# Kernel tuning notes

Hardware: AMD Instinct MI355X
Metric: run time of the kernel (lower is better)

Reference implementation:

```python
import jax, jax.numpy as jnp
import numpy as np

B, L_Q, L_K = 16, 256, 256
Q_DIM, K_DIM, H_DIM, V_DIM = 256, 256, 128, 128


def setup_inputs() -> dict:
    key = jax.random.key(0)
    k1, k2, k3, k4, k5, k6 = jax.random.split(key, 6)
    query = jax.random.normal(k1, (B, L_Q, Q_DIM), dtype=jnp.float32)
    key_t = jax.random.normal(k2, (B, L_K, K_DIM), dtype=jnp.float32)
    value = jax.random.normal(k3, (B, L_Q, V_DIM), dtype=jnp.float32)
    # Linear weights stored as [in, out] for x @ W (equivalent to torch Linear, no bias)
    Wq = jax.random.normal(k4, (Q_DIM, H_DIM), dtype=jnp.float32) / np.sqrt(Q_DIM)
    Wk = jax.random.normal(k5, (K_DIM, H_DIM), dtype=jnp.float32) / np.sqrt(K_DIM)
    v = jax.random.uniform(k6, (H_DIM,), dtype=jnp.float32, minval=-0.1, maxval=0.1)
    return {"query": query, "key": key_t, "value": value, "Wq": Wq, "Wk": Wk, "v": v}


def reference(query, key, value, Wq, Wk, v):
    # Project first (equivalent to applying Linear after the expand, but cheaper):
    qp = jnp.einsum("bqd,dh->bqh", query, Wq)  # [B, l_q, h]
    kp = jnp.einsum("bkd,dh->bkh", key, Wk)    # [B, l_k, h]
    # score[b, k, q] = tanh(qp[b,q] + kp[b,k]) . v  -> [B, l_k, l_q]
    score = jnp.einsum("bkqh,h->bkq", jnp.tanh(qp[:, None, :, :] + kp[:, :, None, :]), v)
    attention = jax.nn.softmax(score, axis=-1)  # softmax over query positions (dim -1)
    context = jnp.einsum("bkq,bqv->bkv", attention, value)  # bmm
    return context, attention
```

## Files before the change

### kernel.cpp

```cpp
#include <hip/hip_runtime.h>

#define B_  16
#define LQ  256
#define LK  256
#define QD  256
#define HD  128
#define VD  128

#define SCALE2 2.8853900817779268f
#define L2E    1.4426950408889634f
#define CTX_SIZE (B_ * LK * VD)

__device__ __forceinline__ float fast_exp2(float x) { return __builtin_amdgcn_exp2f(x); }
__device__ __forceinline__ float fast_rcp(float x)  { return __builtin_amdgcn_rcpf(x); }

__global__ __launch_bounds__(256, 4) void proj_kernel(const float* __restrict__ query,
                                                      const float* __restrict__ key,
                                                      const float* __restrict__ Wq,
                                                      const float* __restrict__ Wk,
                                                      float4* __restrict__ qe4,
                                                      float4* __restrict__ ke4)
{
    __shared__ float  Xs[8][258];
    __shared__ float4 part[4][32][9];

    const int t = threadIdx.x;
    const int xcd = blockIdx.x & 7;
    const int i   = blockIdx.x >> 3;
    const bool isQ = (i < 64);
    const int j    = isQ ? i : (i - 64);
    const int b    = xcd + ((j >> 5) << 3);
    const int rows0 = b * 256 + (j & 31) * 8;

    const float* X = isQ ? query : key;
    const float4* W4 = (const float4*)(isQ ? Wq : Wk);

    {
        const int r = t >> 5;
        const int c = (t & 31) * 8;
        const float4 x0 = *(const float4*)(X + (size_t)(rows0 + r) * QD + c);
        const float4 x1 = *(const float4*)(X + (size_t)(rows0 + r) * QD + c + 4);
        *(float4*)&Xs[r][c]     = x0;
        *(float4*)&Xs[r][c + 4] = x1;
    }
    __syncthreads();

    const int w    = t >> 6;
    const int lane = t & 63;
    const int hg   = lane & 31;
    const int mb   = lane >> 5;

    float4 acc[4];
#pragma unroll
    for (int m = 0; m < 4; m++) acc[m] = make_float4(0.f, 0.f, 0.f, 0.f);

    const int kbase = w * 64;
#pragma unroll 4
    for (int kk = 0; kk < 64; kk += 2) {
        const int k = kbase + kk;
        const float4 w0 = W4[(size_t)k * 32 + hg];
        const float4 w1 = W4[(size_t)(k + 1) * 32 + hg];
#pragma unroll
        for (int mi = 0; mi < 4; mi++) {
            const float2 x = *(const float2*)&Xs[mb + 2 * mi][k];
            acc[mi].x += x.x * w0.x + x.y * w1.x;
            acc[mi].y += x.x * w0.y + x.y * w1.y;
            acc[mi].z += x.x * w0.z + x.y * w1.z;
            acc[mi].w += x.x * w0.w + x.y * w1.w;
        }
    }
#pragma unroll
    for (int mi = 0; mi < 4; mi++) part[w][hg][mb + 2 * mi] = acc[mi];
    __syncthreads();

    if (isQ) {
        const int q8 = t & 7, h4 = t >> 3;
        float4 s = part[0][h4][q8];
        const float4 p1 = part[1][h4][q8];
        const float4 p2 = part[2][h4][q8];
        const float4 p3 = part[3][h4][q8];
        s.x += p1.x + p2.x + p3.x;  s.y += p1.y + p2.y + p3.y;
        s.z += p1.z + p2.z + p3.z;  s.w += p1.w + p2.w + p3.w;
        const float4 e = make_float4(fast_exp2(s.x * SCALE2), fast_exp2(s.y * SCALE2),
                                     fast_exp2(s.z * SCALE2), fast_exp2(s.w * SCALE2));
        const int row = rows0 + q8, bb = row >> 8, q = row & 255;
        qe4[((size_t)bb * 32 + h4) * 256 + q] = e;
    } else {
        const int h4 = t & 31, m = t >> 5;
        float4 s = part[0][h4][m];
        const float4 p1 = part[1][h4][m];
        const float4 p2 = part[2][h4][m];
        const float4 p3 = part[3][h4][m];
        s.x += p1.x + p2.x + p3.x;  s.y += p1.y + p2.y + p3.y;
        s.z += p1.z + p2.z + p3.z;  s.w += p1.w + p2.w + p3.w;
        const float4 e = make_float4(fast_exp2(s.x * SCALE2), fast_exp2(s.y * SCALE2),
                                     fast_exp2(s.z * SCALE2), fast_exp2(s.w * SCALE2));
        ke4[(size_t)(rows0 + m) * 32 + h4] = e;
    }
}

__global__ __launch_bounds__(1024, 8) void score_kernel(const float4* __restrict__ qe4,
                                                        const float4* __restrict__ ke4,
                                                        const float* __restrict__ v,
                                                        float* __restrict__ out)
{
    __shared__ float score_s[8][260];

    const int t   = threadIdx.x;
    const int xcd = blockIdx.x & 7;
    const int i   = blockIdx.x >> 3;
    const int b   = xcd + ((i >> 5) << 3);
    const int k0  = (i & 31) << 3;

    const int kq = t >> 8;
    const int q  = t & 255;

    const float4* qb = qe4 + (size_t)b * 32 * 256;
    const float4* kb = ke4 + ((size_t)b * LK + k0 + kq * 2) * 32;
    const float4* v4 = (const float4*)v;

    float acc0 = 0.f, acc1 = 0.f;
#pragma unroll 4
    for (int h4 = 0; h4 < 32; h4++) {
        const float4 qv = qb[(size_t)h4 * 256 + q];
        const float4 vv = v4[h4];
        const float4 ka = kb[h4];
        const float4 kc = kb[32 + h4];
        acc0 += vv.x * fast_rcp(qv.x * ka.x + 1.f) + vv.y * fast_rcp(qv.y * ka.y + 1.f)
              + vv.z * fast_rcp(qv.z * ka.z + 1.f) + vv.w * fast_rcp(qv.w * ka.w + 1.f);
        acc1 += vv.x * fast_rcp(qv.x * kc.x + 1.f) + vv.y * fast_rcp(qv.y * kc.y + 1.f)
              + vv.z * fast_rcp(qv.z * kc.z + 1.f) + vv.w * fast_rcp(qv.w * kc.w + 1.f);
    }
    float sumv = 0.f;
#pragma unroll
    for (int h4 = 0; h4 < 32; h4++) {
        const float4 vv = v4[h4];
        sumv += vv.x + vv.y + vv.z + vv.w;
    }
    score_s[kq * 2 + 0][q] = sumv - 2.f * acc0;
    score_s[kq * 2 + 1][q] = sumv - 2.f * acc1;
    __syncthreads();

    if (t < 512) {
        const int w = t >> 6, lane = t & 63;
        float x0 = score_s[w][lane];
        float x1 = score_s[w][lane + 64];
        float x2 = score_s[w][lane + 128];
        float x3 = score_s[w][lane + 192];
        float m = fmaxf(fmaxf(x0, x1), fmaxf(x2, x3));
#pragma unroll
        for (int off = 32; off >= 1; off >>= 1) m = fmaxf(m, __shfl_xor(m, off));
        float e0 = fast_exp2((x0 - m) * L2E);
        float e1 = fast_exp2((x1 - m) * L2E);
        float e2 = fast_exp2((x2 - m) * L2E);
        float e3 = fast_exp2((x3 - m) * L2E);
        float s = e0 + e1 + e2 + e3;
#pragma unroll
        for (int off = 32; off >= 1; off >>= 1) s += __shfl_xor(s, off);
        const float rs = fast_rcp(s);
        float* ao = out + CTX_SIZE + ((size_t)(b * LK + k0 + w)) * LQ;
        ao[lane]       = e0 * rs;
        ao[lane + 64]  = e1 * rs;
        ao[lane + 128] = e2 * rs;
        ao[lane + 192] = e3 * rs;
    }
}

__global__ __launch_bounds__(256, 4) void ctx_kernel(const float* __restrict__ value,
                                                     float* __restrict__ out)
{
    __shared__ float  At[8][260];
    __shared__ float4 part[8][8][32];

    const int t   = threadIdx.x;
    const int xcd = blockIdx.x & 7;
    const int i   = blockIdx.x >> 3;
    const int b   = xcd + ((i >> 5) << 3);
    const int k0  = (i & 31) << 3;

    {
        const float* ab = out + CTX_SIZE + ((size_t)(b * LK + k0)) * LQ;
        const int r = t >> 5, c = (t & 31) * 4;
        *(float4*)&At[r][c]       = *(const float4*)(ab + (size_t)r * LQ + c);
        *(float4*)&At[r][c + 128] = *(const float4*)(ab + (size_t)r * LQ + c + 128);
    }
    __syncthreads();

    const int qsub = t >> 5;
    const int vd4  = t & 31;
    const float4* valb = (const float4*)(value + (size_t)b * LQ * VD);

    float4 acc[8];
#pragma unroll
    for (int k = 0; k < 8; k++) acc[k] = make_float4(0.f, 0.f, 0.f, 0.f);

#pragma unroll 4
    for (int iq = 0; iq < 32; iq++) {
        const int q = qsub * 32 + iq;
        const float4 vv = valb[(size_t)q * 32 + vd4];
#pragma unroll
        for (int k = 0; k < 8; k++) {
            const float a = At[k][q];
            acc[k].x += a * vv.x;
            acc[k].y += a * vv.y;
            acc[k].z += a * vv.z;
            acc[k].w += a * vv.w;
        }
    }
#pragma unroll
    for (int k = 0; k < 8; k++) part[qsub][k][vd4] = acc[k];
    __syncthreads();

    {
        const int k = t >> 5, c = t & 31;
        float4 s = part[0][k][c];
#pragma unroll
        for (int qs = 1; qs < 8; qs++) {
            const float4 p = part[qs][k][c];
            s.x += p.x; s.y += p.y; s.z += p.z; s.w += p.w;
        }
        *(float4*)(out + ((size_t)(b * LK + k0 + k)) * VD + c * 4) = s;
    }
}

extern "C" void kernel_launch(void* const* d_in, const int* in_sizes, int n_in,
                              void* d_out, int out_size, void* d_ws, size_t ws_size,
                              hipStream_t stream)
{
    const float* query = (const float*)d_in[0];
    const float* key   = (const float*)d_in[1];
    const float* value = (const float*)d_in[2];
    const float* Wq    = (const float*)d_in[3];
    const float* Wk    = (const float*)d_in[4];
    const float* v     = (const float*)d_in[5];
    float* out = (float*)d_out;

    float4* qe4 = (float4*)d_ws;
    float4* ke4 = qe4 + (size_t)B_ * 32 * 256;

    proj_kernel<<<dim3(1024), 256, 0, stream>>>(query, key, Wq, Wk, qe4, ke4);
    score_kernel<<<dim3(512), 1024, 0, stream>>>(qe4, ke4, v, out);
    ctx_kernel<<<dim3(512), 256, 0, stream>>>(value, out);
}
```

Before: 116.8 us.

## Map one wave per key row in score kernel and fuse softmax in registers

The score kernel now gives each 64-lane wave a full key row, with each lane computing four query positions. Softmax then runs directly on registers through wave shuffles, so the shared-memory staging and block barrier go away. The constant sum(v) is dropped because softmax is shift-invariant, and the max becomes a min over the accumulators with the scale folded into exp2. Launch shape changes from 512 blocks of 1024 threads to 2048 blocks of 128 threads, so the key vector is reused across four query values per lane instead of the query being reused across two keys.

```diff
diff --git a/kernel.cpp b/kernel.cpp
--- a/kernel.cpp
+++ b/kernel.cpp
@@ -8,7 +8,6 @@
 #define VD  128
 
 #define SCALE2 2.8853900817779268f
-#define L2E    1.4426950408889634f
 #define CTX_SIZE (B_ * LK * VD)
 
 __device__ __forceinline__ float fast_exp2(float x) { return __builtin_amdgcn_exp2f(x); }
@@ -99,71 +98,59 @@
     }
 }
 
-__global__ __launch_bounds__(1024, 8) void score_kernel(const float4* __restrict__ qe4,
-                                                        const float4* __restrict__ ke4,
-                                                        const float* __restrict__ v,
-                                                        float* __restrict__ out)
-{
-    __shared__ float score_s[8][260];
-
-    const int t   = threadIdx.x;
-    const int xcd = blockIdx.x & 7;
-    const int i   = blockIdx.x >> 3;
-    const int b   = xcd + ((i >> 5) << 3);
-    const int k0  = (i & 31) << 3;
-
-    const int kq = t >> 8;
-    const int q  = t & 255;
+__global__ __launch_bounds__(128, 8) void score_kernel(const float4* __restrict__ qe4,
+                                                       const float4* __restrict__ ke4,
+                                                       const float* __restrict__ v,
+                                                       float* __restrict__ out)
+{
+    const int t    = threadIdx.x;
+    const int wv   = t >> 6;
+    const int lane = t & 63;
+    const int xcd  = blockIdx.x & 7;
+    const int r    = blockIdx.x >> 3;
+    const int b    = xcd + ((r & 1) << 3);
+    const int k    = (r >> 1) * 2 + wv;
 
     const float4* qb = qe4 + (size_t)b * 32 * 256;
-    const float4* kb = ke4 + ((size_t)b * LK + k0 + kq * 2) * 32;
+    const float4* kb = ke4 + ((size_t)b * LK + k) * 32;
     const float4* v4 = (const float4*)v;
 
-    float acc0 = 0.f, acc1 = 0.f;
-#pragma unroll 4
+    float acc0 = 0.f, acc1 = 0.f, acc2 = 0.f, acc3 = 0.f;
+#pragma unroll 2
     for (int h4 = 0; h4 < 32; h4++) {
-        const float4 qv = qb[(size_t)h4 * 256 + q];
+        const float4 kv = kb[h4];
         const float4 vv = v4[h4];
-        const float4 ka = kb[h4];
-        const float4 kc = kb[32 + h4];
-        acc0 += vv.x * fast_rcp(qv.x * ka.x + 1.f) + vv.y * fast_rcp(qv.y * ka.y + 1.f)
-              + vv.z * fast_rcp(qv.z * ka.z + 1.f) + vv.w * fast_rcp(qv.w * ka.w + 1.f);
-        acc1 += vv.x * fast_rcp(qv.x * kc.x + 1.f) + vv.y * fast_rcp(qv.y * kc.y + 1.f)
-              + vv.z * fast_rcp(qv.z * kc.z + 1.f) + vv.w * fast_rcp(qv.w * kc.w + 1.f);
-    }
-    float sumv = 0.f;
-#pragma unroll
-    for (int h4 = 0; h4 < 32; h4++) {
-        const float4 vv = v4[h4];
-        sumv += vv.x + vv.y + vv.z + vv.w;
-    }
-    score_s[kq * 2 + 0][q] = sumv - 2.f * acc0;
-    score_s[kq * 2 + 1][q] = sumv - 2.f * acc1;
-    __syncthreads();
-
-    if (t < 512) {
-        const int w = t >> 6, lane = t & 63;
-        float x0 = score_s[w][lane];
-        float x1 = score_s[w][lane + 64];
-        float x2 = score_s[w][lane + 128];
-        float x3 = score_s[w][lane + 192];
-        float m = fmaxf(fmaxf(x0, x1), fmaxf(x2, x3));
-#pragma unroll
-        for (int off = 32; off >= 1; off >>= 1) m = fmaxf(m, __shfl_xor(m, off));
-        float e0 = fast_exp2((x0 - m) * L2E);
-        float e1 = fast_exp2((x1 - m) * L2E);
-        float e2 = fast_exp2((x2 - m) * L2E);
-        float e3 = fast_exp2((x3 - m) * L2E);
-        float s = e0 + e1 + e2 + e3;
-#pragma unroll
-        for (int off = 32; off >= 1; off >>= 1) s += __shfl_xor(s, off);
-        const float rs = fast_rcp(s);
-        float* ao = out + CTX_SIZE + ((size_t)(b * LK + k0 + w)) * LQ;
-        ao[lane]       = e0 * rs;
-        ao[lane + 64]  = e1 * rs;
-        ao[lane + 128] = e2 * rs;
-        ao[lane + 192] = e3 * rs;
-    }
+        const float4 q0 = qb[(size_t)h4 * 256 + lane];
+        const float4 q1 = qb[(size_t)h4 * 256 + lane + 64];
+        const float4 q2 = qb[(size_t)h4 * 256 + lane + 128];
+        const float4 q3 = qb[(size_t)h4 * 256 + lane + 192];
+        acc0 += vv.x * fast_rcp(q0.x * kv.x + 1.f) + vv.y * fast_rcp(q0.y * kv.y + 1.f)
+              + vv.z * fast_rcp(q0.z * kv.z + 1.f) + vv.w * fast_rcp(q0.w * kv.w + 1.f);
+        acc1 += vv.x * fast_rcp(q1.x * kv.x + 1.f) + vv.y * fast_rcp(q1.y * kv.y + 1.f)
+              + vv.z * fast_rcp(q1.z * kv.z + 1.f) + vv.w * fast_rcp(q1.w * kv.w + 1.f);
+        acc2 += vv.x * fast_rcp(q2.x * kv.x + 1.f) + vv.y * fast_rcp(q2.y * kv.y + 1.f)
+              + vv.z * fast_rcp(q2.z * kv.z + 1.f) + vv.w * fast_rcp(q2.w * kv.w + 1.f);
+        acc3 += vv.x * fast_rcp(q3.x * kv.x + 1.f) + vv.y * fast_rcp(q3.y * kv.y + 1.f)
+              + vv.z * fast_rcp(q3.z * kv.z + 1.f) + vv.w * fast_rcp(q3.w * kv.w + 1.f);
+    }
+
+    float amin = fminf(fminf(acc0, acc1), fminf(acc2, acc3));
+#pragma unroll
+    for (int off = 32; off >= 1; off >>= 1) amin = fminf(amin, __shfl_xor(amin, off));
+    const float e0 = fast_exp2(-SCALE2 * (acc0 - amin));
+    const float e1 = fast_exp2(-SCALE2 * (acc1 - amin));
+    const float e2 = fast_exp2(-SCALE2 * (acc2 - amin));
+    const float e3 = fast_exp2(-SCALE2 * (acc3 - amin));
+    float s = e0 + e1 + e2 + e3;
+#pragma unroll
+    for (int off = 32; off >= 1; off >>= 1) s += __shfl_xor(s, off);
+    const float rs = fast_rcp(s);
+
+    float* ao = out + CTX_SIZE + ((size_t)(b * LK + k)) * LQ;
+    ao[lane]       = e0 * rs;
+    ao[lane + 64]  = e1 * rs;
+    ao[lane + 128] = e2 * rs;
+    ao[lane + 192] = e3 * rs;
 }
 
 __global__ __launch_bounds__(256, 4) void ctx_kernel(const float* __restrict__ value,
@@ -239,6 +226,6 @@
     float4* ke4 = qe4 + (size_t)B_ * 32 * 256;
 
     proj_kernel<<<dim3(1024), 256, 0, stream>>>(query, key, Wq, Wk, qe4, ke4);
-    score_kernel<<<dim3(512), 1024, 0, stream>>>(qe4, ke4, v, out);
+    score_kernel<<<dim3(2048), 128, 0, stream>>>(qe4, ke4, v, out);
     ctx_kernel<<<dim3(512), 256, 0, stream>>>(value, out);
 }
```

Measured after the change: 111.8 us. 4.2% less time.
